# Kernel tuning notes

Hardware: AMD Instinct MI355X
Metric: run time of the kernel (lower is better)

The kernel has to match this reference:

```python
import jax, jax.numpy as jnp
import numpy as np

H, HK, HD = 6, 2, 128  # n_heads, n_kv_heads, head_dim (from AcousticTransformerArgs defaults)


def setup_inputs() -> dict:
    key = jax.random.key(0)
    k1, k2, k3, k4, k5 = jax.random.split(key, 5)
    B, S, D = 2, 4096, 768
    s = 0.02
    return {
        "x": jax.random.normal(k1, (B, S, D), dtype=jnp.float32),
        "wq": jax.random.normal(k2, (H * HD, D), dtype=jnp.float32) * s,
        "wk": jax.random.normal(k3, (HK * HD, D), dtype=jnp.float32) * s,
        "wv": jax.random.normal(k4, (HK * HD, D), dtype=jnp.float32) * s,
        "wo": jax.random.normal(k5, (D, H * HD), dtype=jnp.float32) * s,
    }


def reference(x, wq, wk, wv, wo):
    B, S, D = x.shape
    rep = H // HK  # GQA repeat factor (3)
    scale = 1.0 / jnp.sqrt(jnp.asarray(HD, x.dtype))
    # projections (torch Linear: y = x @ W^T)
    q = (x @ wq.T).reshape(B, S, HK, rep, HD) * scale  # head h = g*rep + r
    k = (x @ wk.T).reshape(B, S, HK, HD)
    v = (x @ wv.T).reshape(B, S, HK, HD)
    # bidirectional (no mask) attention with GQA broadcast instead of physical repeat
    scores = jnp.einsum("bsgrd,btgd->bgrst", q, k)  # [B,HK,rep,S,S]
    attn = jax.nn.softmax(scores, axis=-1)
    out = jnp.einsum("bgrst,btgd->bsgrd", attn, v).reshape(B, S, H * HD)
    return out @ wo.T
```

## Files before the change

kernel.cpp:

```cpp
#include <hip/hip_runtime.h>
#include <hip/hip_bf16.h>
#include <type_traits>

using bf16 = __hip_bfloat16;
typedef __attribute__((ext_vector_type(8))) short bf16x8;
typedef __attribute__((ext_vector_type(4))) float floatx4;

static constexpr int Bb = 2, S = 4096, D = 768, H = 6, HK = 2, HD = 128, REP = 3;
static constexpr int M_ROWS = Bb * S;
static constexpr int NQKV = 1280;

__device__ __forceinline__ floatx4 mfma16(bf16x8 a, bf16x8 b, floatx4 c) {
  return __builtin_amdgcn_mfma_f32_16x16x32_bf16(a, b, c, 0, 0, 0);
}

__device__ __forceinline__ void gld_lds16(const bf16* g, bf16* l) {
  __builtin_amdgcn_global_load_lds(
      (const __attribute__((address_space(1))) unsigned int*)g,
      (__attribute__((address_space(3))) unsigned int*)l, 16, 0, 0);
}

#if defined(__has_builtin)
#if __has_builtin(__builtin_amdgcn_exp2f)
#define EXP2F(x) __builtin_amdgcn_exp2f(x)
#endif
#endif
#ifndef EXP2F
#define EXP2F(x) exp2f(x)
#endif

__device__ __forceinline__ unsigned pk2(float a, float b) {
  unsigned ua = __builtin_bit_cast(unsigned, a) + 0x8000u;
  unsigned ub = __builtin_bit_cast(unsigned, b) + 0x8000u;
#if defined(__has_builtin) && __has_builtin(__builtin_amdgcn_perm)
  return __builtin_amdgcn_perm(ub, ua, 0x07060302);
#else
  return (ua >> 16) | (ub & 0xffff0000u);
#endif
}

__global__ __launch_bounds__(256) void cvt_bf16(const float* __restrict__ in,
                                                bf16* __restrict__ out, int n, float scale) {
  int i = blockIdx.x * 256 + threadIdx.x;
  if (i < n) out[i] = __float2bfloat16(in[i] * scale);
}

template <typename OutT>
__global__ __launch_bounds__(256) void gemm_bt(const bf16* __restrict__ A,
                                               const bf16* __restrict__ W,
                                               OutT* __restrict__ C, int M, int N, int K) {
  const int tid = threadIdx.x;
  const int wave = tid >> 6, lane = tid & 63;
  const int quad = lane >> 4, lq = lane & 15;
  const int m0 = blockIdx.x * 128, n0 = blockIdx.y * 128;
  const int wm = (wave & 1) * 64, wn = (wave >> 1) * 64;

  __shared__ __align__(16) bf16 As[128 * 32];
  __shared__ __align__(16) bf16 Ws[128 * 32];

  floatx4 acc[4][4] = {};

  const int srow = lane >> 2, sc = lane & 3;

  for (int k0 = 0; k0 < K; k0 += 32) {
#pragma unroll
    for (int i = 0; i < 2; ++i) {
      int ig = wave * 2 + i;
      int r = ig * 16 + srow;
      int c = sc ^ ((r >> 1) & 3);
      gld_lds16(&A[(size_t)(m0 + r) * K + k0 + c * 8], &As[ig * 512]);
      gld_lds16(&W[(size_t)(n0 + r) * K + k0 + c * 8], &Ws[ig * 512]);
    }
    __syncthreads();
    bf16x8 af[4], wf[4];
#pragma unroll
    for (int i = 0; i < 4; ++i) {
      int ra = wm + i * 16 + lq, rw = wn + i * 16 + lq;
      af[i] = *(const bf16x8*)&As[ra * 32 + ((quad ^ ((ra >> 1) & 3)) * 8)];
      wf[i] = *(const bf16x8*)&Ws[rw * 32 + ((quad ^ ((rw >> 1) & 3)) * 8)];
    }
#pragma unroll
    for (int i = 0; i < 4; ++i)
#pragma unroll
      for (int j = 0; j < 4; ++j) acc[i][j] = mfma16(af[i], wf[j], acc[i][j]);
    __syncthreads();
  }
#pragma unroll
  for (int i = 0; i < 4; ++i)
#pragma unroll
    for (int j = 0; j < 4; ++j)
#pragma unroll
      for (int r = 0; r < 4; ++r) {
        int row = m0 + wm + i * 16 + quad * 4 + r;
        int col = n0 + wn + j * 16 + lq;
        float v = acc[i][j][r];
        if constexpr (std::is_same_v<OutT, float>)
          C[(size_t)row * N + col] = v;
        else
          C[(size_t)row * N + col] = __float2bfloat16(v);
      }
}

__global__ __launch_bounds__(256) void transpose_v(const bf16* __restrict__ QKV,
                                                   bf16* __restrict__ Vt) {
  __shared__ bf16 t[32][33];
  int bg = blockIdx.z;
  int b = bg >> 1, g = bg & 1;
  int t0 = blockIdx.x * 32, d0 = blockIdx.y * 32;
  int tx = threadIdx.x, ty = threadIdx.y;
  for (int i = 0; i < 32; i += 8)
    t[ty + i][tx] = QKV[((size_t)b * S + t0 + ty + i) * NQKV + (H * HD + HK * HD) + g * HD + d0 + tx];
  __syncthreads();
  for (int i = 0; i < 32; i += 8)
    Vt[((size_t)(b * HK + g) * HD + d0 + ty + i) * S + t0 + tx] = t[tx][ty + i];
}

__global__ __launch_bounds__(256, 2) void flash_attn(const bf16* __restrict__ QKV,
                                                     const bf16* __restrict__ Vt,
                                                     bf16* __restrict__ O) {
  const int bid = blockIdx.x;
  const int bg = (bid & 7) >> 1;
  const int b = bg >> 1, g = bg & 1;
  const int qt = ((bid >> 3) << 1) | (bid & 1);
  const int q0 = qt * 32;

  const int tid = threadIdx.x;
  const int w = tid >> 6, lane = tid & 63;
  const int half = w >> 1, wp = w & 1;
  const int quad = lane >> 4, lq = lane & 15;

  __shared__ __align__(16) char smem[77824];
  bf16* Ks = (bf16*)smem;
  bf16* Vs = (bf16*)(smem + 32768);
  bf16* Pt = (bf16*)(smem + 65536);

  const bf16* Kgh = QKV + (size_t)b * S * NQKV + H * HD + g * HD + (size_t)half * 2048 * NQKV;
  const bf16* Vgh = Vt + (size_t)(b * HK + g) * HD * S + half * 2048;

  auto stage = [&](int t0, int buf) {
    bf16* kd = Ks + (buf * 2 + half) * 4096;
    bf16* vd = Vs + (buf * 2 + half) * 4096;
#pragma unroll
    for (int i = 0; i < 4; ++i) {
      int ig = wp * 4 + i;
      int tl = ig * 4 + (lane >> 4);
      int c = (lane & 15) ^ (tl & 15);
      gld_lds16(Kgh + (size_t)(t0 + tl) * NQKV + c * 8, kd + ig * 512);
    }
#pragma unroll
    for (int i = 0; i < 4; ++i) {
      int ig = wp * 4 + i;
      int dl = ig * 16 + (lane >> 2);
      int c = (lane & 3) ^ ((dl >> 1) & 3);
      gld_lds16(Vgh + (size_t)dl * S + t0 + c * 8, vd + ig * 512);
    }
  };

  stage(0, 0);

  const bf16* Qg = QKV + ((size_t)b * S + q0 + wp * 16 + lq) * NQKV + g * REP * HD;
  bf16x8 qf[3][4];
#pragma unroll
  for (int u = 0; u < 3; ++u)
#pragma unroll
    for (int kk = 0; kk < 4; ++kk)
      qf[u][kk] = *(const bf16x8*)(Qg + u * HD + kk * 32 + quad * 8);

  floatx4 o[3][8] = {};
  float lp[3] = {0.f, 0.f, 0.f};
  const int sw = (lq >> 1) & 3;

  for (int it = 0; it < 64; ++it) {
    const int cur = it & 1;
    __syncthreads();
    if (it + 1 < 64) stage((it + 1) * 32, cur ^ 1);

    const bf16* ks = Ks + (cur * 2 + half) * 4096;
    const bf16* vs = Vs + (cur * 2 + half) * 4096;

    floatx4 sf[3][2] = {};
#pragma unroll
    for (int tt = 0; tt < 2; ++tt)
#pragma unroll
      for (int kk = 0; kk < 4; ++kk) {
        int c = (kk * 4 + quad) ^ lq;
        bf16x8 kf = *(const bf16x8*)&ks[(tt * 16 + lq) * 128 + c * 8];
#pragma unroll
        for (int u = 0; u < 3; ++u) sf[u][tt] = mfma16(kf, qf[u][kk], sf[u][tt]);
      }

#pragma unroll
    for (int u = 0; u < 3; ++u) {
      char* ptb = (char*)(Pt + (w * 3 + u) * 512);
#pragma unroll
      for (int tt = 0; tt < 2; ++tt) {
        float p0 = EXP2F(sf[u][tt][0]), p1 = EXP2F(sf[u][tt][1]);
        float p2 = EXP2F(sf[u][tt][2]), p3 = EXP2F(sf[u][tt][3]);
        lp[u] += (p0 + p1) + (p2 + p3);
        uint2 pkv;
        pkv.x = pk2(p0, p1);
        pkv.y = pk2(p2, p3);
        int cc = (tt * 2 + (quad >> 1)) ^ sw;
        *(uint2*)(ptb + lq * 64 + cc * 16 + (quad & 1) * 8) = pkv;
      }
    }

    bf16x8 pf[3];
#pragma unroll
    for (int u = 0; u < 3; ++u) {
      const char* ptb = (const char*)(Pt + (w * 3 + u) * 512);
      pf[u] = *(const bf16x8*)(ptb + lq * 64 + ((quad ^ sw) * 16));
    }

#pragma unroll
    for (int dd = 0; dd < 8; ++dd) {
      bf16x8 vf = *(const bf16x8*)&vs[(dd * 16 + lq) * 32 + ((quad ^ sw) * 8)];
#pragma unroll
      for (int u = 0; u < 3; ++u) o[u][dd] = mfma16(vf, pf[u], o[u][dd]);
    }
  }

  __syncthreads();
  floatx4* oscr = (floatx4*)smem;
  float* lscr = (float*)(smem + 49152);
  if (half == 1) {
#pragma unroll
    for (int u = 0; u < 3; ++u) {
#pragma unroll
      for (int dd = 0; dd < 8; ++dd)
        oscr[((wp * 3 + u) * 8 + dd) * 64 + lane] = o[u][dd];
      lscr[(wp * 3 + u) * 64 + lane] = lp[u];
    }
  }
  __syncthreads();
  if (half == 0) {
    const size_t row = (size_t)b * S + q0 + wp * 16 + lq;
#pragma unroll
    for (int u = 0; u < 3; ++u) {
      float l = lp[u] + lscr[(wp * 3 + u) * 64 + lane];
      l += __shfl_xor(l, 16);
      l += __shfl_xor(l, 32);
      float rinv = 1.0f / l;
#pragma unroll
      for (int dd = 0; dd < 8; ++dd) {
        floatx4 oc = o[u][dd] + oscr[((wp * 3 + u) * 8 + dd) * 64 + lane];
        uint2 st;
        st.x = pk2(oc[0] * rinv, oc[1] * rinv);
        st.y = pk2(oc[2] * rinv, oc[3] * rinv);
        int col = (g * REP + u) * HD + dd * 16 + quad * 4;
        *(uint2*)&O[row * (H * HD) + col] = st;
      }
    }
  }
}

static inline size_t al256(size_t x) { return (x + 255) & ~size_t(255); }

extern "C" void kernel_launch(void* const* d_in, const int* in_sizes, int n_in,
                              void* d_out, int out_size, void* d_ws, size_t ws_size,
                              hipStream_t stream) {
  const float* x  = (const float*)d_in[0];
  const float* wq = (const float*)d_in[1];
  const float* wk = (const float*)d_in[2];
  const float* wv = (const float*)d_in[3];
  const float* wo = (const float*)d_in[4];
  float* out = (float*)d_out;

  char* w = (char*)d_ws;
  size_t off = 0;
  auto carve = [&](size_t elems) {
    bf16* p = (bf16*)(w + off);
    off = al256(off + elems * sizeof(bf16));
    return p;
  };
  bf16* xb    = carve((size_t)M_ROWS * D);
  bf16* wqkvb = carve((size_t)NQKV * D);
  bf16* wob   = carve((size_t)D * (H * HD));
  bf16* QKVb  = carve((size_t)M_ROWS * NQKV);
  bf16* Vtb   = carve((size_t)M_ROWS * (HK * HD));
  bf16* Ab    = carve((size_t)M_ROWS * (H * HD));

  const float qscale = 0.1275174465f;

  auto cvt = [&](const float* in, bf16* o2, int n, float s) {
    cvt_bf16<<<(n + 255) / 256, 256, 0, stream>>>(in, o2, n, s);
  };
  cvt(x, xb, M_ROWS * D, 1.f);
  cvt(wq, wqkvb, H * HD * D, qscale);
  cvt(wk, wqkvb + (size_t)(H * HD) * D, HK * HD * D, 1.f);
  cvt(wv, wqkvb + (size_t)(H * HD + HK * HD) * D, HK * HD * D, 1.f);
  cvt(wo, wob, D * H * HD, 1.f);

  gemm_bt<bf16><<<dim3(M_ROWS / 128, NQKV / 128), 256, 0, stream>>>(
      xb, wqkvb, QKVb, M_ROWS, NQKV, D);

  transpose_v<<<dim3(S / 32, HD / 32, Bb * HK), dim3(32, 8), 0, stream>>>(QKVb, Vtb);

  flash_attn<<<512, 256, 0, stream>>>(QKVb, Vtb, Ab);

  gemm_bt<float><<<dim3(M_ROWS / 128, D / 128), 256, 0, stream>>>(
      Ab, wob, out, M_ROWS, D, H * HD);
}
```

Before: 249.6 us.

## Fuse conversions, fold V transpose into QKV GEMM, widen GEMM K-tile, MFMA row sums

Replaces the five per-tensor conversion launches with one vectorized cvt_all kernel. The QKV GEMM now writes the V columns directly in transposed layout, which removes the separate transpose kernel and its extra pass over memory. The GEMM K-tile is doubled to 64 with a new XOR swizzle, halving the barrier count per K step. In flash attention, the softmax denominator is accumulated with an MFMA against a ones vector instead of scalar adds and shuffles, and the main loop is unrolled by 2. This costs more LDS and registers, and the transposed V stores from the GEMM are strided 8-byte writes.

```diff
diff --git a/kernel.cpp b/kernel.cpp
--- a/kernel.cpp
+++ b/kernel.cpp
@@ -39,51 +39,98 @@
 #endif
 }
 
-__global__ __launch_bounds__(256) void cvt_bf16(const float* __restrict__ in,
-                                                bf16* __restrict__ out, int n, float scale) {
-  int i = blockIdx.x * 256 + threadIdx.x;
-  if (i < n) out[i] = __float2bfloat16(in[i] * scale);
-}
-
-template <typename OutT>
+static constexpr size_t E_X  = (size_t)M_ROWS * D;
+static constexpr size_t E_WQ = E_X + (size_t)H * HD * D;
+static constexpr size_t E_WK = E_WQ + (size_t)HK * HD * D;
+static constexpr size_t E_WV = E_WK + (size_t)HK * HD * D;
+static constexpr size_t E_WO = E_WV + (size_t)D * H * HD;
+
+__global__ __launch_bounds__(256) void cvt_all(const float* __restrict__ x,
+                                               const float* __restrict__ wq,
+                                               const float* __restrict__ wk,
+                                               const float* __restrict__ wv,
+                                               const float* __restrict__ wo,
+                                               bf16* __restrict__ xb,
+                                               bf16* __restrict__ wqkvb,
+                                               bf16* __restrict__ wob, float qscale) {
+  size_t i = ((size_t)blockIdx.x * 256 + threadIdx.x) * 4;
+  const float* src;
+  bf16* dst;
+  float s = 1.f;
+  size_t off;
+  if (i < E_X)        { src = x;  dst = xb;                 off = i; }
+  else if (i < E_WQ)  { src = wq; dst = wqkvb;              off = i - E_X; s = qscale; }
+  else if (i < E_WK)  { src = wk; dst = wqkvb + 589824;     off = i - E_WQ; }
+  else if (i < E_WV)  { src = wv; dst = wqkvb + 786432;     off = i - E_WK; }
+  else                { src = wo; dst = wob;                off = i - E_WV; }
+  float4 v = *(const float4*)(src + off);
+  uint2 st;
+  st.x = pk2(v.x * s, v.y * s);
+  st.y = pk2(v.z * s, v.w * s);
+  *(uint2*)(dst + off) = st;
+}
+
+template <typename OutT, bool VT_FUSE>
 __global__ __launch_bounds__(256) void gemm_bt(const bf16* __restrict__ A,
                                                const bf16* __restrict__ W,
-                                               OutT* __restrict__ C, int M, int N, int K) {
+                                               OutT* __restrict__ C,
+                                               bf16* __restrict__ Vt,
+                                               int M, int N, int K) {
   const int tid = threadIdx.x;
   const int wave = tid >> 6, lane = tid & 63;
   const int quad = lane >> 4, lq = lane & 15;
   const int m0 = blockIdx.x * 128, n0 = blockIdx.y * 128;
   const int wm = (wave & 1) * 64, wn = (wave >> 1) * 64;
 
-  __shared__ __align__(16) bf16 As[128 * 32];
-  __shared__ __align__(16) bf16 Ws[128 * 32];
+  __shared__ __align__(16) bf16 As[128 * 64];
+  __shared__ __align__(16) bf16 Ws[128 * 64];
 
   floatx4 acc[4][4] = {};
 
-  const int srow = lane >> 2, sc = lane & 3;
-
-  for (int k0 = 0; k0 < K; k0 += 32) {
-#pragma unroll
-    for (int i = 0; i < 2; ++i) {
-      int ig = wave * 2 + i;
-      int r = ig * 16 + srow;
-      int c = sc ^ ((r >> 1) & 3);
+  const int srow = lane >> 3, sc = lane & 7;
+
+  for (int k0 = 0; k0 < K; k0 += 64) {
+#pragma unroll
+    for (int i = 0; i < 4; ++i) {
+      int ig = wave * 4 + i;
+      int r = ig * 8 + srow;
+      int c = sc ^ (r & 7);
       gld_lds16(&A[(size_t)(m0 + r) * K + k0 + c * 8], &As[ig * 512]);
       gld_lds16(&W[(size_t)(n0 + r) * K + k0 + c * 8], &Ws[ig * 512]);
     }
     __syncthreads();
-    bf16x8 af[4], wf[4];
-#pragma unroll
-    for (int i = 0; i < 4; ++i) {
-      int ra = wm + i * 16 + lq, rw = wn + i * 16 + lq;
-      af[i] = *(const bf16x8*)&As[ra * 32 + ((quad ^ ((ra >> 1) & 3)) * 8)];
-      wf[i] = *(const bf16x8*)&Ws[rw * 32 + ((quad ^ ((rw >> 1) & 3)) * 8)];
-    }
+#pragma unroll
+    for (int kh = 0; kh < 2; ++kh) {
+      bf16x8 af[4], wf[4];
+#pragma unroll
+      for (int i = 0; i < 4; ++i) {
+        int ra = wm + i * 16 + lq, rw = wn + i * 16 + lq;
+        af[i] = *(const bf16x8*)&As[ra * 64 + (((kh * 4 + quad) ^ (ra & 7)) * 8)];
+        wf[i] = *(const bf16x8*)&Ws[rw * 64 + (((kh * 4 + quad) ^ (rw & 7)) * 8)];
+      }
+#pragma unroll
+      for (int i = 0; i < 4; ++i)
+#pragma unroll
+        for (int j = 0; j < 4; ++j) acc[i][j] = mfma16(af[i], wf[j], acc[i][j]);
+    }
+    __syncthreads();
+  }
+
+  if (VT_FUSE && n0 >= 1024) {
+    const int b = m0 >> 12;
 #pragma unroll
     for (int i = 0; i < 4; ++i)
 #pragma unroll
-      for (int j = 0; j < 4; ++j) acc[i][j] = mfma16(af[i], wf[j], acc[i][j]);
-    __syncthreads();
+      for (int j = 0; j < 4; ++j) {
+        int col = n0 + wn + j * 16 + lq - 1024;
+        int gg = col >> 7, dd = col & 127;
+        int s = (m0 + wm + i * 16 + quad * 4) & 4095;
+        uint2 st;
+        st.x = pk2(acc[i][j][0], acc[i][j][1]);
+        st.y = pk2(acc[i][j][2], acc[i][j][3]);
+        *(uint2*)&Vt[(((size_t)(b * HK + gg) * HD + dd) * S) + s] = st;
+      }
+    return;
   }
 #pragma unroll
   for (int i = 0; i < 4; ++i)
@@ -101,20 +148,6 @@
       }
 }
 
-__global__ __launch_bounds__(256) void transpose_v(const bf16* __restrict__ QKV,
-                                                   bf16* __restrict__ Vt) {
-  __shared__ bf16 t[32][33];
-  int bg = blockIdx.z;
-  int b = bg >> 1, g = bg & 1;
-  int t0 = blockIdx.x * 32, d0 = blockIdx.y * 32;
-  int tx = threadIdx.x, ty = threadIdx.y;
-  for (int i = 0; i < 32; i += 8)
-    t[ty + i][tx] = QKV[((size_t)b * S + t0 + ty + i) * NQKV + (H * HD + HK * HD) + g * HD + d0 + tx];
-  __syncthreads();
-  for (int i = 0; i < 32; i += 8)
-    Vt[((size_t)(b * HK + g) * HD + d0 + ty + i) * S + t0 + tx] = t[tx][ty + i];
-}
-
 __global__ __launch_bounds__(256, 2) void flash_attn(const bf16* __restrict__ QKV,
                                                      const bf16* __restrict__ Vt,
                                                      bf16* __restrict__ O) {
@@ -166,10 +199,15 @@
     for (int kk = 0; kk < 4; ++kk)
       qf[u][kk] = *(const bf16x8*)(Qg + u * HD + kk * 32 + quad * 8);
 
+  bf16x8 ones;
+#pragma unroll
+  for (int j = 0; j < 8; ++j) ones[j] = (short)0x3F80;
+
   floatx4 o[3][8] = {};
-  float lp[3] = {0.f, 0.f, 0.f};
+  floatx4 lacc[3] = {};
   const int sw = (lq >> 1) & 3;
 
+#pragma unroll 2
   for (int it = 0; it < 64; ++it) {
     const int cur = it & 1;
     __syncthreads();
@@ -196,7 +234,6 @@
       for (int tt = 0; tt < 2; ++tt) {
         float p0 = EXP2F(sf[u][tt][0]), p1 = EXP2F(sf[u][tt][1]);
         float p2 = EXP2F(sf[u][tt][2]), p3 = EXP2F(sf[u][tt][3]);
-        lp[u] += (p0 + p1) + (p2 + p3);
         uint2 pkv;
         pkv.x = pk2(p0, p1);
         pkv.y = pk2(p2, p3);
@@ -213,6 +250,9 @@
     }
 
 #pragma unroll
+    for (int u = 0; u < 3; ++u) lacc[u] = mfma16(ones, pf[u], lacc[u]);
+
+#pragma unroll
     for (int dd = 0; dd < 8; ++dd) {
       bf16x8 vf = *(const bf16x8*)&vs[(dd * 16 + lq) * 32 + ((quad ^ sw) * 8)];
 #pragma unroll
@@ -229,7 +269,7 @@
 #pragma unroll
       for (int dd = 0; dd < 8; ++dd)
         oscr[((wp * 3 + u) * 8 + dd) * 64 + lane] = o[u][dd];
-      lscr[(wp * 3 + u) * 64 + lane] = lp[u];
+      lscr[(wp * 3 + u) * 64 + lane] = lacc[u][0];
     }
   }
   __syncthreads();
@@ -237,9 +277,7 @@
     const size_t row = (size_t)b * S + q0 + wp * 16 + lq;
 #pragma unroll
     for (int u = 0; u < 3; ++u) {
-      float l = lp[u] + lscr[(wp * 3 + u) * 64 + lane];
-      l += __shfl_xor(l, 16);
-      l += __shfl_xor(l, 32);
+      float l = lacc[u][0] + lscr[(wp * 3 + u) * 64 + lane];
       float rinv = 1.0f / l;
 #pragma unroll
       for (int dd = 0; dd < 8; ++dd) {
@@ -282,22 +320,13 @@
 
   const float qscale = 0.1275174465f;
 
-  auto cvt = [&](const float* in, bf16* o2, int n, float s) {
-    cvt_bf16<<<(n + 255) / 256, 256, 0, stream>>>(in, o2, n, s);
-  };
-  cvt(x, xb, M_ROWS * D, 1.f);
-  cvt(wq, wqkvb, H * HD * D, qscale);
-  cvt(wk, wqkvb + (size_t)(H * HD) * D, HK * HD * D, 1.f);
-  cvt(wv, wqkvb + (size_t)(H * HD + HK * HD) * D, HK * HD * D, 1.f);
-  cvt(wo, wob, D * H * HD, 1.f);
-
-  gemm_bt<bf16><<<dim3(M_ROWS / 128, NQKV / 128), 256, 0, stream>>>(
-      xb, wqkvb, QKVb, M_ROWS, NQKV, D);
-
-  transpose_v<<<dim3(S / 32, HD / 32, Bb * HK), dim3(32, 8), 0, stream>>>(QKVb, Vtb);
+  cvt_all<<<(int)(E_WO / 1024), 256, 0, stream>>>(x, wq, wk, wv, wo, xb, wqkvb, wob, qscale);
+
+  gemm_bt<bf16, true><<<dim3(M_ROWS / 128, NQKV / 128), 256, 0, stream>>>(
+      xb, wqkvb, QKVb, Vtb, M_ROWS, NQKV, D);
 
   flash_attn<<<512, 256, 0, stream>>>(QKVb, Vtb, Ab);
 
-  gemm_bt<float><<<dim3(M_ROWS / 128, D / 128), 256, 0, stream>>>(
-      Ab, wob, out, M_ROWS, D, H * HD);
-}
+  gemm_bt<float, false><<<dim3(M_ROWS / 128, D / 128), 256, 0, stream>>>(
+      Ab, wob, out, nullptr, M_ROWS, D, H * HD);
+}
```

After: 234.8 us. -5.9%, faster.
